# Optimization experiments

Hardware: AMD Instinct MI355X
Metric: run time of the kernel (lower is better)

## Reference

```python
import jax, jax.numpy as jnp
import numpy as np

N_NODES = 100000
N_EDGES = 1600000
D_IN = 128
D_HID = 128
D_OUT = 64


def setup_inputs() -> dict:
    key = jax.random.key(0)
    ks = jax.random.split(key, 7)
    x = jax.random.normal(ks[0], (N_NODES, D_IN), dtype=jnp.float32)
    edge_index = jax.random.randint(ks[1], (2, N_EDGES), 0, N_NODES, dtype=jnp.int64)
    s = 1.0 / np.sqrt(D_IN)
    Wl1 = jax.random.normal(ks[2], (D_IN, D_HID), dtype=jnp.float32) * s
    Wr1 = jax.random.normal(ks[3], (D_IN, D_HID), dtype=jnp.float32) * s
    b1 = jnp.zeros((D_HID,), dtype=jnp.float32)
    s2 = 1.0 / np.sqrt(D_HID)
    Wl2 = jax.random.normal(ks[4], (D_HID, D_OUT), dtype=jnp.float32) * s2
    Wr2 = jax.random.normal(ks[5], (D_HID, D_OUT), dtype=jnp.float32) * s2
    b2 = jnp.zeros((D_OUT,), dtype=jnp.float32)
    return {"x": x, "edge_index": edge_index, "Wl1": Wl1, "Wr1": Wr1, "b1": b1,
            "Wl2": Wl2, "Wr2": Wr2, "b2": b2}


def _sage_conv(x, src, dst, Wl, Wr, b, n_nodes):
    # PyG SAGEConv, aggr='mean': out = lin_l(mean_{j in N(i)} x_j) + lin_r(x_i)
    msg = x[src]                                              # [E, D] gather
    agg = jax.ops.segment_sum(msg, dst, num_segments=n_nodes) # [N, D] scatter-add
    cnt = jax.ops.segment_sum(jnp.ones((src.shape[0],), x.dtype), dst,
                              num_segments=n_nodes)           # [N] in-degree
    agg = agg / jnp.maximum(cnt, 1.0)[:, None]                # mean (0 for isolated)
    return agg @ Wl + x @ Wr + b


def reference(x, edge_index, Wl1, Wr1, b1, Wl2, Wr2, b2):
    src, dst = edge_index[0], edge_index[1]  # source_to_target flow
    n = x.shape[0]
    h = jax.nn.relu(_sage_conv(x, src, dst, Wl1, Wr1, b1, n))
    out = _sage_conv(h, src, dst, Wl2, Wr2, b2, n)
    return out
```

## Files before the change

### kernel.cpp

```cpp
#include <hip/hip_runtime.h>


constexpr int TPB = 256;
constexpr int CAP = 64;
constexpr int NBIN = 256;
constexpr int NBLKA = 512;

typedef __attribute__((ext_vector_type(8))) short bf16x8;
typedef __attribute__((ext_vector_type(4))) float f32x4;

static __device__ __forceinline__ unsigned short f2bf(float f) {
    unsigned int u = __float_as_uint(f);
    u += 0x7fffu + ((u >> 16) & 1u);
    return (unsigned short)(u >> 16);
}
static __device__ __forceinline__ float bfe2f(short s) {
    return __uint_as_float(((unsigned int)(unsigned short)s) << 16);
}


__global__ void binA_count(const int* __restrict__ dst, int* __restrict__ blockhist,
                           int E, int epb) {
    __shared__ int hist[NBIN];
    hist[threadIdx.x] = 0;
    __syncthreads();
    int e0 = blockIdx.x * epb, e1 = min(E, e0 + epb);
    for (int i = e0 + threadIdx.x; i < e1; i += TPB)
        atomicAdd(&hist[dst[i] >> 9], 1);
    __syncthreads();
    blockhist[threadIdx.x * NBLKA + blockIdx.x] = hist[threadIdx.x];
}

__global__ void binA_total(const int* __restrict__ blockhist, int* __restrict__ bintotal) {
    __shared__ int s[TPB];
    int b = blockIdx.x;
    int sum = 0;
    for (int i = threadIdx.x; i < NBLKA; i += TPB) sum += blockhist[b * NBLKA + i];
    s[threadIdx.x] = sum;
    __syncthreads();
    for (int o = 128; o > 0; o >>= 1) {
        if (threadIdx.x < o) s[threadIdx.x] += s[threadIdx.x + o];
        __syncthreads();
    }
    if (threadIdx.x == 0) bintotal[b] = s[0];
}

__global__ void binA_scan(const int* __restrict__ bintotal, int* __restrict__ binstart) {
    __shared__ int s[NBIN];
    int t = threadIdx.x;
    s[t] = bintotal[t];
    __syncthreads();
    for (int o = 1; o < NBIN; o <<= 1) {
        int v = (t >= o) ? s[t - o] : 0;
        __syncthreads();
        s[t] += v;
        __syncthreads();
    }
    binstart[t] = t ? s[t - 1] : 0;
    if (t == NBIN - 1) binstart[NBIN] = s[NBIN - 1];
}

__global__ void binA_boff(const int* __restrict__ blockhist, const int* __restrict__ binstart,
                          int* __restrict__ boff) {
    __shared__ int s[NBLKA];
    int b = blockIdx.x, t = threadIdx.x;
    s[t] = blockhist[b * NBLKA + t];
    __syncthreads();
    for (int o = 1; o < NBLKA; o <<= 1) {
        int v = (t >= o) ? s[t - o] : 0;
        __syncthreads();
        s[t] += v;
        __syncthreads();
    }
    int excl = t ? s[t - 1] : 0;
    boff[b * NBLKA + t] = binstart[b] + excl;
}

__global__ void binA_scatter(const int* __restrict__ src, const int* __restrict__ dst,
                             const int* __restrict__ boff, int2* __restrict__ sorted,
                             int E, int epb) {
    __shared__ int base[NBIN];
    __shared__ int lcur[NBIN];
    int t = threadIdx.x, blk = blockIdx.x;
    base[t] = boff[t * NBLKA + blk];
    lcur[t] = 0;
    __syncthreads();
    int e0 = blk * epb, e1 = min(E, e0 + epb);
    for (int i = e0 + t; i < e1; i += TPB) {
        int d = dst[i];
        int b = d >> 9;
        int p = base[b] + atomicAdd(&lcur[b], 1);
        sorted[p] = make_int2(src[i], d);
    }
}

__global__ void binB_build(const int2* __restrict__ sorted, const int* __restrict__ binstart,
                           int* __restrict__ cursor, int* __restrict__ nbrp, int N) {
    __shared__ int lcur[512];
    int t = threadIdx.x, b = blockIdx.x;
    lcur[t] = 0;
    lcur[t + 256] = 0;
    __syncthreads();
    int lo = binstart[b], hi = binstart[b + 1];
    int node0 = b << 9;
    for (int i = lo + t; i < hi; i += TPB) {
        int2 e = sorted[i];
        int p = atomicAdd(&lcur[e.y - node0], 1);
        if (p < CAP) nbrp[(size_t)e.y * CAP + p] = e.x;
    }
    __syncthreads();
    for (int k = t; k < 512; k += TPB) {
        int node = node0 + k;
        if (node < N) cursor[node] = lcur[k];
    }
}

__global__ void cast_bf16_kernel(const float* __restrict__ in, unsigned short* __restrict__ out,
                                 int n4) {
    int i = blockIdx.x * TPB + threadIdx.x;
    if (i < n4) {
        float4 v = ((const float4*)in)[i];
        ushort4 o;
        o.x = f2bf(v.x); o.y = f2bf(v.y); o.z = f2bf(v.z); o.w = f2bf(v.w);
        ((ushort4*)out)[i] = o;
    }
}

__global__ void weight_prep_kernel(const float* __restrict__ Wl1, const float* __restrict__ Wr1,
                                   const float* __restrict__ Wl2, const float* __restrict__ Wr2,
                                   unsigned short* __restrict__ Wt1,
                                   unsigned short* __restrict__ Wt2a,
                                   unsigned short* __restrict__ Wt2b) {
    int idx = blockIdx.x * TPB + threadIdx.x;
    if (idx < 128 * 256) {
        int co = idx & 127, k = idx >> 7;
        float v = (k < 128) ? Wl1[k * 128 + co] : Wr1[(k - 128) * 128 + co];
        Wt1[(size_t)co * 256 + k] = f2bf(v);
    } else if (idx < 128 * 256 + 64 * 128) {
        int j = idx - 128 * 256;
        int co = j & 63, k = j >> 6;
        Wt2a[(size_t)co * 128 + k] = f2bf(Wl2[k * 64 + co]);
    } else if (idx < 128 * 256 + 2 * 64 * 128) {
        int j = idx - 128 * 256 - 64 * 128;
        int co = j & 63, k = j >> 6;
        Wt2b[(size_t)co * 128 + k] = f2bf(Wr2[k * 64 + co]);
    }
}

template <int D, bool FINALADD>
__global__ __launch_bounds__(256) void gather_mean_kernel(
    const unsigned short* __restrict__ feat,
    const int* __restrict__ nbrp,
    const int* __restrict__ cursor,
    const float* __restrict__ ub,
    void* __restrict__ outv,
    int N) {
    constexpr int LPN = D / 8;
    int gid = blockIdx.x * TPB + threadIdx.x;
    int node = gid / LPN;
    if (node >= N) return;
    const int lane = threadIdx.x & 63;
    const int part = lane & (LPN - 1);
    const int base = lane & ~(LPN - 1);
    const unsigned short* fcol = feat + part * 8;

    const int* lst = nbrp + (size_t)node * CAP;
    int dtrue = cursor[node];
    int d = min(dtrue, CAP);

    int id0 = lst[part];
    int id1 = lst[LPN + part];
    int id2 = 0, id3 = 0;
    if (LPN == 8) {
        id2 = lst[2 * LPN + part];
        id3 = lst[3 * LPN + part];
    }

    float a0[8], a1[8], a2[8], a3[8];
#pragma unroll
    for (int i = 0; i < 8; i++) { a0[i] = 0.f; a1[i] = 0.f; a2[i] = 0.f; a3[i] = 0.f; }

#pragma unroll
    for (int c = 0; c < 8; c++) {
        const int j = c * 4;
        const int blk = (LPN == 8) ? (j >> 3) : (j >> 4);
        int sel = (blk == 0) ? id0 : (blk == 1) ? id1 : (blk == 2) ? id2 : id3;
        const int sl = base + (j & (LPN - 1));
        int s0 = __shfl(sel, sl + 0);
        int s1 = __shfl(sel, sl + 1);
        int s2 = __shfl(sel, sl + 2);
        int s3 = __shfl(sel, sl + 3);
        float w0 = (j + 0 < d) ? 1.f : 0.f;
        float w1 = (j + 1 < d) ? 1.f : 0.f;
        float w2 = (j + 2 < d) ? 1.f : 0.f;
        float w3 = (j + 3 < d) ? 1.f : 0.f;
        s0 = (j + 0 < d) ? s0 : 0;
        s1 = (j + 1 < d) ? s1 : 0;
        s2 = (j + 2 < d) ? s2 : 0;
        s3 = (j + 3 < d) ? s3 : 0;
        bf16x8 v0 = *(const bf16x8*)(fcol + (size_t)s0 * D);
        bf16x8 v1 = *(const bf16x8*)(fcol + (size_t)s1 * D);
        bf16x8 v2 = *(const bf16x8*)(fcol + (size_t)s2 * D);
        bf16x8 v3 = *(const bf16x8*)(fcol + (size_t)s3 * D);
#pragma unroll
        for (int i = 0; i < 8; i++) {
            a0[i] = fmaf(w0, bfe2f(v0[i]), a0[i]);
            a1[i] = fmaf(w1, bfe2f(v1[i]), a1[i]);
            a2[i] = fmaf(w2, bfe2f(v2[i]), a2[i]);
            a3[i] = fmaf(w3, bfe2f(v3[i]), a3[i]);
        }
    }
    for (int j = 32; j < d; j++) {
        int s0 = lst[j];
        bf16x8 v0 = *(const bf16x8*)(fcol + (size_t)s0 * D);
#pragma unroll
        for (int i = 0; i < 8; i++) a0[i] += bfe2f(v0[i]);
    }

    float sc = 1.0f / (float)max(dtrue, 1);
    float r[8];
#pragma unroll
    for (int i = 0; i < 8; i++) r[i] = (a0[i] + a1[i] + a2[i] + a3[i]) * sc;

    if (FINALADD) {
        const float* up = ub + (size_t)node * D + part * 8;
        float* op = (float*)outv + (size_t)node * D + part * 8;
        float4 u0 = *(const float4*)(up);
        float4 u1 = *(const float4*)(up + 4);
        float4 o0 = make_float4(r[0] + u0.x, r[1] + u0.y, r[2] + u0.z, r[3] + u0.w);
        float4 o1 = make_float4(r[4] + u1.x, r[5] + u1.y, r[6] + u1.z, r[7] + u1.w);
        *(float4*)(op) = o0;
        *(float4*)(op + 4) = o1;
    } else {
        bf16x8 st;
#pragma unroll
        for (int i = 0; i < 8; i++) st[i] = (short)f2bf(r[i]);
        *(bf16x8*)((unsigned short*)outv + (size_t)node * D + part * 8) = st;
    }
}

__global__ __launch_bounds__(256) void sage1_mfma_kernel(
    const unsigned short* __restrict__ A1,
    const unsigned short* __restrict__ A2,
    const unsigned short* __restrict__ Wt,
    const float* __restrict__ bias,
    unsigned short* __restrict__ outb,
    int N, int ntiles) {
    constexpr int K = 256, KS = 8;

    const int tid = threadIdx.x;
    const int lane = tid & 63;
    const int wave = tid >> 6;
    const int lrow = lane & 15;
    const int kb = (lane >> 4) * 8;
    const int colgrp = wave & 1;
    const int mslot = wave >> 1;
    const int colbase = colgrp * 64;

    bf16x8 B[4][KS];
#pragma unroll
    for (int t = 0; t < 4; t++)
#pragma unroll
        for (int ks = 0; ks < KS; ks++)
            B[t][ks] = *(const bf16x8*)(Wt + (size_t)(colbase + t * 16 + lrow) * K + ks * 32 + kb);

    for (int tile = blockIdx.x * 2 + mslot; tile < ntiles; tile += gridDim.x * 2) {
        const int m0 = tile * 16;
        const int arow = min(m0 + lrow, N - 1);

        bf16x8 a[KS];
#pragma unroll
        for (int ks = 0; ks < KS; ks++) {
            if (ks >= 4)
                a[ks] = *(const bf16x8*)(A2 + (size_t)arow * 128 + (ks - 4) * 32 + kb);
            else
                a[ks] = *(const bf16x8*)(A1 + (size_t)arow * 128 + ks * 32 + kb);
        }

        f32x4 acc[4];
#pragma unroll
        for (int t = 0; t < 4; t++) acc[t] = (f32x4){0.f, 0.f, 0.f, 0.f};
#pragma unroll
        for (int ks = 0; ks < KS; ks++)
#pragma unroll
            for (int t = 0; t < 4; t++)
                acc[t] = __builtin_amdgcn_mfma_f32_16x16x32_bf16(a[ks], B[t][ks], acc[t], 0, 0, 0);

        const int mb = m0 + (lane >> 4) * 4;
#pragma unroll
        for (int t = 0; t < 4; t++) {
            const int col = colbase + t * 16 + lrow;
            const float bv = bias[col];
#pragma unroll
            for (int r = 0; r < 4; r++) {
                const int m = mb + r;
                if (m < N) {
                    float v = fmaxf(acc[t][r] + bv, 0.f);
                    outb[(size_t)m * 128 + col] = f2bf(v);
                }
            }
        }
    }
}

__global__ __launch_bounds__(256) void gemm64_dual_kernel(
    const unsigned short* __restrict__ h,
    const unsigned short* __restrict__ Wta,
    const unsigned short* __restrict__ Wtb,
    const float* __restrict__ bias,
    unsigned short* __restrict__ tb,
    float* __restrict__ ub,
    int N, int ntiles) {
    constexpr int K = 128, KS = 4;

    const int tid = threadIdx.x;
    const int lane = tid & 63;
    const int wave = tid >> 6;
    const int lrow = lane & 15;
    const int kb = (lane >> 4) * 8;

    bf16x8 Ba[4][KS], Bb[4][KS];
#pragma unroll
    for (int t = 0; t < 4; t++)
#pragma unroll
        for (int ks = 0; ks < KS; ks++) {
            Ba[t][ks] = *(const bf16x8*)(Wta + (size_t)(t * 16 + lrow) * K + ks * 32 + kb);
            Bb[t][ks] = *(const bf16x8*)(Wtb + (size_t)(t * 16 + lrow) * K + ks * 32 + kb);
        }

    for (int tile = blockIdx.x * 4 + wave; tile < ntiles; tile += gridDim.x * 4) {
        const int m0 = tile * 16;
        const int arow = min(m0 + lrow, N - 1);

        bf16x8 a[KS];
#pragma unroll
        for (int ks = 0; ks < KS; ks++)
            a[ks] = *(const bf16x8*)(h + (size_t)arow * 128 + ks * 32 + kb);

        f32x4 acct[4], accu[4];
#pragma unroll
        for (int t = 0; t < 4; t++) {
            acct[t] = (f32x4){0.f, 0.f, 0.f, 0.f};
            accu[t] = (f32x4){0.f, 0.f, 0.f, 0.f};
        }
#pragma unroll
        for (int ks = 0; ks < KS; ks++)
#pragma unroll
            for (int t = 0; t < 4; t++) {
                acct[t] = __builtin_amdgcn_mfma_f32_16x16x32_bf16(a[ks], Ba[t][ks], acct[t], 0, 0, 0);
                accu[t] = __builtin_amdgcn_mfma_f32_16x16x32_bf16(a[ks], Bb[t][ks], accu[t], 0, 0, 0);
            }

        const int mb = m0 + (lane >> 4) * 4;
#pragma unroll
        for (int t = 0; t < 4; t++) {
            const int col = t * 16 + lrow;
            const float bv = bias[col];
#pragma unroll
            for (int r = 0; r < 4; r++) {
                const int m = mb + r;
                if (m < N) {
                    tb[(size_t)m * 64 + col] = f2bf(acct[t][r]);
                    ub[(size_t)m * 64 + col] = accu[t][r] + bv;
                }
            }
        }
    }
}

extern "C" void kernel_launch(void* const* d_in, const int* in_sizes, int n_in,
                              void* d_out, int out_size, void* d_ws, size_t ws_size,
                              hipStream_t stream) {
    const float* x   = (const float*)d_in[0];
    const int* ei    = (const int*)d_in[1];
    const float* Wl1 = (const float*)d_in[2];
    const float* Wr1 = (const float*)d_in[3];
    const float* b1  = (const float*)d_in[4];
    const float* Wl2 = (const float*)d_in[5];
    const float* Wr2 = (const float*)d_in[6];
    const float* b2  = (const float*)d_in[7];
    float* out = (float*)d_out;

    const int N = in_sizes[0] / 128;
    const int E = in_sizes[1] / 2;
    const int* src = ei;
    const int* dst = ei + E;

    const int epb = (E + NBLKA - 1) / NBLKA;
    const int ntiles = (N + 15) / 16;
    const int nNodeBins = (N + 511) >> 9;

    unsigned short* xb = (unsigned short*)d_out;
    float* ub          = (float*)d_out;

    unsigned short* h    = (unsigned short*)d_ws;
    unsigned short* aggb = h + (size_t)N * 128;
    int2* sorted         = (int2*)aggb;
    unsigned short* tb   = aggb + (size_t)N * 128;
    unsigned short* Wt1  = tb + (size_t)N * 64;
    unsigned short* Wt2a = Wt1 + 128 * 256;
    unsigned short* Wt2b = Wt2a + 64 * 128;
    int* cursor    = (int*)(Wt2b + 64 * 128);
    int* nbrp      = cursor + N;
    int* blockhist = nbrp + (size_t)N * CAP;
    int* bintotal  = blockhist + NBIN * NBLKA;
    int* binstart  = bintotal + NBIN;
    int* boff      = binstart + (NBIN + 1);

    weight_prep_kernel<<<(128 * 256 + 2 * 64 * 128 + TPB - 1) / TPB, TPB, 0, stream>>>(
        Wl1, Wr1, Wl2, Wr2, Wt1, Wt2a, Wt2b);
    binA_count<<<NBLKA, TPB, 0, stream>>>(dst, blockhist, E, epb);
    binA_total<<<NBIN, TPB, 0, stream>>>(blockhist, bintotal);
    binA_scan<<<1, NBIN, 0, stream>>>(bintotal, binstart);
    binA_boff<<<NBIN, NBLKA, 0, stream>>>(blockhist, binstart, boff);
    binA_scatter<<<NBLKA, TPB, 0, stream>>>(src, dst, boff, sorted, E, epb);
    binB_build<<<nNodeBins, TPB, 0, stream>>>(sorted, binstart, cursor, nbrp, N);

    cast_bf16_kernel<<<((N * 128 / 4) + TPB - 1) / TPB, TPB, 0, stream>>>(x, xb, N * 128 / 4);
    gather_mean_kernel<128, false><<<(N * 16 + TPB - 1) / TPB, TPB, 0, stream>>>(
        xb, nbrp, cursor, nullptr, aggb, N);
    sage1_mfma_kernel<<<512, 256, 0, stream>>>(aggb, xb, Wt1, b1, h, N, ntiles);

    gemm64_dual_kernel<<<512, 256, 0, stream>>>(h, Wt2a, Wt2b, b2, tb, ub, N, ntiles);
    gather_mean_kernel<64, true><<<(N * 8 + TPB - 1) / TPB, TPB, 0, stream>>>(
        tb, nbrp, cursor, ub, out, N);
}
```

Before: 200.8 us.

## Gather neighbor features in FP8 instead of BF16 for both mean aggregations

Result: faster. 178.6 us (-11.0%).

```diff
diff --git a/kernel.cpp b/kernel.cpp
--- a/kernel.cpp
+++ b/kernel.cpp
@@ -13,9 +13,6 @@
     unsigned int u = __float_as_uint(f);
     u += 0x7fffu + ((u >> 16) & 1u);
     return (unsigned short)(u >> 16);
-}
-static __device__ __forceinline__ float bfe2f(short s) {
-    return __uint_as_float(((unsigned int)(unsigned short)s) << 16);
 }
 
 
@@ -115,14 +112,18 @@
     }
 }
 
-__global__ void cast_bf16_kernel(const float* __restrict__ in, unsigned short* __restrict__ out,
-                                 int n4) {
+__global__ void cast_kernel(const float* __restrict__ in, unsigned short* __restrict__ outb,
+                            unsigned char* __restrict__ outq, int n4) {
     int i = blockIdx.x * TPB + threadIdx.x;
     if (i < n4) {
         float4 v = ((const float4*)in)[i];
         ushort4 o;
         o.x = f2bf(v.x); o.y = f2bf(v.y); o.z = f2bf(v.z); o.w = f2bf(v.w);
-        ((ushort4*)out)[i] = o;
+        ((ushort4*)outb)[i] = o;
+        int p = 0;
+        p = __builtin_amdgcn_cvt_pk_fp8_f32(v.x, v.y, p, false);
+        p = __builtin_amdgcn_cvt_pk_fp8_f32(v.z, v.w, p, true);
+        ((int*)outq)[i] = p;
     }
 }
 
@@ -149,93 +150,109 @@
 
 template <int D, bool FINALADD>
 __global__ __launch_bounds__(256) void gather_mean_kernel(
-    const unsigned short* __restrict__ feat,
+    const unsigned char* __restrict__ feat,
     const int* __restrict__ nbrp,
     const int* __restrict__ cursor,
     const float* __restrict__ ub,
     void* __restrict__ outv,
     int N) {
-    constexpr int LPN = D / 8;
+    constexpr int LPN = D / 16;
+    constexpr int NID = 32 / LPN;
     int gid = blockIdx.x * TPB + threadIdx.x;
     int node = gid / LPN;
     if (node >= N) return;
     const int lane = threadIdx.x & 63;
     const int part = lane & (LPN - 1);
     const int base = lane & ~(LPN - 1);
-    const unsigned short* fcol = feat + part * 8;
-
-    const int* lst = nbrp + (size_t)node * CAP;
+    const unsigned pb = (unsigned)(part * 16);
+
+    const int* lst = nbrp + (unsigned)(node * CAP);
     int dtrue = cursor[node];
     int d = min(dtrue, CAP);
-
-    int id0 = lst[part];
-    int id1 = lst[LPN + part];
-    int id2 = 0, id3 = 0;
-    if (LPN == 8) {
-        id2 = lst[2 * LPN + part];
-        id3 = lst[3 * LPN + part];
-    }
-
-    float a0[8], a1[8], a2[8], a3[8];
-#pragma unroll
-    for (int i = 0; i < 8; i++) { a0[i] = 0.f; a1[i] = 0.f; a2[i] = 0.f; a3[i] = 0.f; }
+    int d32 = min(d, 32);
+
+    int ids[NID];
+#pragma unroll
+    for (int k = 0; k < NID; k++) ids[k] = lst[k * LPN + part];
+
+    float a[16], b[16];
+#pragma unroll
+    for (int i = 0; i < 16; i++) { a[i] = 0.f; b[i] = 0.f; }
 
 #pragma unroll
     for (int c = 0; c < 8; c++) {
-        const int j = c * 4;
-        const int blk = (LPN == 8) ? (j >> 3) : (j >> 4);
-        int sel = (blk == 0) ? id0 : (blk == 1) ? id1 : (blk == 2) ? id2 : id3;
-        const int sl = base + (j & (LPN - 1));
-        int s0 = __shfl(sel, sl + 0);
-        int s1 = __shfl(sel, sl + 1);
-        int s2 = __shfl(sel, sl + 2);
-        int s3 = __shfl(sel, sl + 3);
-        float w0 = (j + 0 < d) ? 1.f : 0.f;
-        float w1 = (j + 1 < d) ? 1.f : 0.f;
-        float w2 = (j + 2 < d) ? 1.f : 0.f;
-        float w3 = (j + 3 < d) ? 1.f : 0.f;
-        s0 = (j + 0 < d) ? s0 : 0;
-        s1 = (j + 1 < d) ? s1 : 0;
-        s2 = (j + 2 < d) ? s2 : 0;
-        s3 = (j + 3 < d) ? s3 : 0;
-        bf16x8 v0 = *(const bf16x8*)(fcol + (size_t)s0 * D);
-        bf16x8 v1 = *(const bf16x8*)(fcol + (size_t)s1 * D);
-        bf16x8 v2 = *(const bf16x8*)(fcol + (size_t)s2 * D);
-        bf16x8 v3 = *(const bf16x8*)(fcol + (size_t)s3 * D);
+        int sj[4];
+        float wj[4];
+#pragma unroll
+        for (int q = 0; q < 4; q++) {
+            const int j = c * 4 + q;
+            int s = __shfl(ids[j / LPN], base + (j & (LPN - 1)));
+            wj[q] = (j < d32) ? 1.f : 0.f;
+            sj[q] = (j < d32) ? s : 0;
+        }
+        int4 v0 = *(const int4*)(feat + ((unsigned)(sj[0] * D) + pb));
+        int4 v1 = *(const int4*)(feat + ((unsigned)(sj[1] * D) + pb));
+        int4 v2 = *(const int4*)(feat + ((unsigned)(sj[2] * D) + pb));
+        int4 v3 = *(const int4*)(feat + ((unsigned)(sj[3] * D) + pb));
+#pragma unroll
+        for (int q = 0; q < 4; q++) {
+            int4 vv = (q == 0) ? v0 : (q == 1) ? v1 : (q == 2) ? v2 : v3;
+            float* acc = (q & 1) ? b : a;
+            const float w = wj[q];
+            int words[4] = {vv.x, vv.y, vv.z, vv.w};
+#pragma unroll
+            for (int t = 0; t < 4; t++) {
+                auto lo = __builtin_amdgcn_cvt_pk_f32_fp8(words[t], false);
+                auto hi = __builtin_amdgcn_cvt_pk_f32_fp8(words[t], true);
+                acc[t * 4 + 0] = fmaf(w, lo[0], acc[t * 4 + 0]);
+                acc[t * 4 + 1] = fmaf(w, lo[1], acc[t * 4 + 1]);
+                acc[t * 4 + 2] = fmaf(w, hi[0], acc[t * 4 + 2]);
+                acc[t * 4 + 3] = fmaf(w, hi[1], acc[t * 4 + 3]);
+            }
+        }
+    }
+    for (int j = 32; j < d; j++) {
+        int4 vv = *(const int4*)(feat + ((unsigned)(lst[j] * D) + pb));
+        int words[4] = {vv.x, vv.y, vv.z, vv.w};
+#pragma unroll
+        for (int t = 0; t < 4; t++) {
+            auto lo = __builtin_amdgcn_cvt_pk_f32_fp8(words[t], false);
+            auto hi = __builtin_amdgcn_cvt_pk_f32_fp8(words[t], true);
+            a[t * 4 + 0] += lo[0];
+            a[t * 4 + 1] += lo[1];
+            a[t * 4 + 2] += hi[0];
+            a[t * 4 + 3] += hi[1];
+        }
+    }
+
+    float sc = 1.0f / (float)max(dtrue, 1);
+    float r[16];
+#pragma unroll
+    for (int i = 0; i < 16; i++) r[i] = (a[i] + b[i]) * sc;
+
+    if (FINALADD) {
+        const float* up = ub + (unsigned)(node * D) + part * 16;
+        float* op = (float*)outv + (unsigned)(node * D) + part * 16;
+#pragma unroll
+        for (int g = 0; g < 4; g++) {
+            float4 u = *(const float4*)(up + g * 4);
+            float4 o;
+            o.x = r[g * 4 + 0] + u.x;
+            o.y = r[g * 4 + 1] + u.y;
+            o.z = r[g * 4 + 2] + u.z;
+            o.w = r[g * 4 + 3] + u.w;
+            *(float4*)(op + g * 4) = o;
+        }
+    } else {
+        unsigned short* op = (unsigned short*)outv + (unsigned)(node * D) + part * 16;
+        bf16x8 s0, s1;
 #pragma unroll
         for (int i = 0; i < 8; i++) {
-            a0[i] = fmaf(w0, bfe2f(v0[i]), a0[i]);
-            a1[i] = fmaf(w1, bfe2f(v1[i]), a1[i]);
-            a2[i] = fmaf(w2, bfe2f(v2[i]), a2[i]);
-            a3[i] = fmaf(w3, bfe2f(v3[i]), a3[i]);
-        }
-    }
-    for (int j = 32; j < d; j++) {
-        int s0 = lst[j];
-        bf16x8 v0 = *(const bf16x8*)(fcol + (size_t)s0 * D);
-#pragma unroll
-        for (int i = 0; i < 8; i++) a0[i] += bfe2f(v0[i]);
-    }
-
-    float sc = 1.0f / (float)max(dtrue, 1);
-    float r[8];
-#pragma unroll
-    for (int i = 0; i < 8; i++) r[i] = (a0[i] + a1[i] + a2[i] + a3[i]) * sc;
-
-    if (FINALADD) {
-        const float* up = ub + (size_t)node * D + part * 8;
-        float* op = (float*)outv + (size_t)node * D + part * 8;
-        float4 u0 = *(const float4*)(up);
-        float4 u1 = *(const float4*)(up + 4);
-        float4 o0 = make_float4(r[0] + u0.x, r[1] + u0.y, r[2] + u0.z, r[3] + u0.w);
-        float4 o1 = make_float4(r[4] + u1.x, r[5] + u1.y, r[6] + u1.z, r[7] + u1.w);
-        *(float4*)(op) = o0;
-        *(float4*)(op + 4) = o1;
-    } else {
-        bf16x8 st;
-#pragma unroll
-        for (int i = 0; i < 8; i++) st[i] = (short)f2bf(r[i]);
-        *(bf16x8*)((unsigned short*)outv + (size_t)node * D + part * 8) = st;
+            s0[i] = (short)f2bf(r[i]);
+            s1[i] = (short)f2bf(r[8 + i]);
+        }
+        *(bf16x8*)(op) = s0;
+        *(bf16x8*)(op + 8) = s1;
     }
 }
 
@@ -308,7 +325,7 @@
     const unsigned short* __restrict__ Wta,
     const unsigned short* __restrict__ Wtb,
     const float* __restrict__ bias,
-    unsigned short* __restrict__ tb,
+    unsigned char* __restrict__ tb,
     float* __restrict__ ub,
     int N, int ntiles) {
     constexpr int K = 128, KS = 4;
@@ -360,7 +377,8 @@
             for (int r = 0; r < 4; r++) {
                 const int m = mb + r;
                 if (m < N) {
-                    tb[(size_t)m * 64 + col] = f2bf(acct[t][r]);
+                    int p = __builtin_amdgcn_cvt_pk_fp8_f32(acct[t][r], acct[t][r], 0, false);
+                    tb[(size_t)m * 64 + col] = (unsigned char)(p & 0xff);
                     ub[(size_t)m * 64 + col] = accu[t][r] + bv;
                 }
             }
@@ -393,19 +411,21 @@
     unsigned short* xb = (unsigned short*)d_out;
     float* ub          = (float*)d_out;
 
-    unsigned short* h    = (unsigned short*)d_ws;
-    unsigned short* aggb = h + (size_t)N * 128;
+    unsigned char* wsb = (unsigned char*)d_ws;
+    unsigned short* h    = (unsigned short*)wsb;              wsb += (size_t)N * 128 * 2;
+    unsigned short* aggb = (unsigned short*)wsb;              wsb += (size_t)N * 128 * 2;
     int2* sorted         = (int2*)aggb;
-    unsigned short* tb   = aggb + (size_t)N * 128;
-    unsigned short* Wt1  = tb + (size_t)N * 64;
-    unsigned short* Wt2a = Wt1 + 128 * 256;
-    unsigned short* Wt2b = Wt2a + 64 * 128;
-    int* cursor    = (int*)(Wt2b + 64 * 128);
-    int* nbrp      = cursor + N;
-    int* blockhist = nbrp + (size_t)N * CAP;
-    int* bintotal  = blockhist + NBIN * NBLKA;
-    int* binstart  = bintotal + NBIN;
-    int* boff      = binstart + (NBIN + 1);
+    unsigned char* tb8   = wsb;                               wsb += (size_t)N * 64;
+    unsigned char* xq    = wsb;                               wsb += (size_t)N * 128;
+    unsigned short* Wt1  = (unsigned short*)wsb;              wsb += 128 * 256 * 2;
+    unsigned short* Wt2a = (unsigned short*)wsb;              wsb += 64 * 128 * 2;
+    unsigned short* Wt2b = (unsigned short*)wsb;              wsb += 64 * 128 * 2;
+    int* cursor    = (int*)wsb;                               wsb += (size_t)N * 4;
+    int* nbrp      = (int*)wsb;                               wsb += (size_t)N * CAP * 4;
+    int* blockhist = (int*)wsb;                               wsb += NBIN * NBLKA * 4;
+    int* bintotal  = (int*)wsb;                               wsb += NBIN * 4;
+    int* binstart  = (int*)wsb;                               wsb += (NBIN + 1) * 4;
+    int* boff      = (int*)wsb;
 
     weight_prep_kernel<<<(128 * 256 + 2 * 64 * 128 + TPB - 1) / TPB, TPB, 0, stream>>>(
         Wl1, Wr1, Wl2, Wr2, Wt1, Wt2a, Wt2b);
@@ -416,12 +436,12 @@
     binA_scatter<<<NBLKA, TPB, 0, stream>>>(src, dst, boff, sorted, E, epb);
     binB_build<<<nNodeBins, TPB, 0, stream>>>(sorted, binstart, cursor, nbrp, N);
 
-    cast_bf16_kernel<<<((N * 128 / 4) + TPB - 1) / TPB, TPB, 0, stream>>>(x, xb, N * 128 / 4);
-    gather_mean_kernel<128, false><<<(N * 16 + TPB - 1) / TPB, TPB, 0, stream>>>(
-        xb, nbrp, cursor, nullptr, aggb, N);
+    cast_kernel<<<((N * 128 / 4) + TPB - 1) / TPB, TPB, 0, stream>>>(x, xb, xq, N * 128 / 4);
+    gather_mean_kernel<128, false><<<(N * 8 + TPB - 1) / TPB, TPB, 0, stream>>>(
+        xq, nbrp, cursor, nullptr, aggb, N);
     sage1_mfma_kernel<<<512, 256, 0, stream>>>(aggb, xb, Wt1, b1, h, N, ntiles);
 
-    gemm64_dual_kernel<<<512, 256, 0, stream>>>(h, Wt2a, Wt2b, b2, tb, ub, N, ntiles);
-    gather_mean_kernel<64, true><<<(N * 8 + TPB - 1) / TPB, TPB, 0, stream>>>(
-        tb, nbrp, cursor, ub, out, N);
-}
+    gemm64_dual_kernel<<<512, 256, 0, stream>>>(h, Wt2a, Wt2b, b2, tb8, ub, N, ntiles);
+    gather_mean_kernel<64, true><<<(N * 4 + TPB - 1) / TPB, TPB, 0, stream>>>(
+        tb8, nbrp, cursor, ub, out, N);
+}
```
